# Kernel optimization log

Hardware: AMD Instinct MI355X
Metric: run time of the kernel (lower is better)

## Reference

```python
import jax, jax.numpy as jnp
import numpy as np


def setup_inputs() -> dict:
    key = jax.random.key(0)
    ks = jax.random.split(key, 8)
    B, I, H, O, K = 4096, 512, 512, 512, 16
    s = 0.02
    return {
        "sample": jax.random.normal(ks[0], (B, I), jnp.float32),
        "hiddens": jax.random.normal(ks[1], (K, B, H), jnp.float32),
        "mem_para": jax.random.uniform(ks[2], (B, H), jnp.float32),
        "Wu": jax.random.normal(ks[3], (I + H, H), jnp.float32) * s,
        "bu": jnp.zeros((H,), jnp.float32),
        "Wr": jax.random.normal(ks[4], (I + H, H), jnp.float32) * s,
        "br": jnp.zeros((H,), jnp.float32),
        "Wm": jax.random.normal(ks[5], (I + 2 * H, H), jnp.float32) * s,
        "bm": jnp.zeros((H,), jnp.float32),
        "Wh": jax.random.normal(ks[6], (I + H, H), jnp.float32) * s,
        "bh": jnp.zeros((H,), jnp.float32),
        "Wo": jax.random.normal(ks[7], (H, O), jnp.float32) * s,
        "bo": jnp.zeros((O,), jnp.float32),
    }


def _mem_filter(hiddens, mem_para):
    # hiddens: [k, B, H]; mem_para (memory gate output, 'd'): [B, H]
    # Original per-scalar recurrence: w[k]=1; w[k-1-i] = w[k-i]*(i-d)/(i+1)
    # => w[k-1-i] = cumprod_{m=0..i} (m-d)/(m+1), i.e. signed fractional binomials.
    k = hiddens.shape[0]
    i = jnp.arange(k, dtype=hiddens.dtype)[:, None, None]          # [k,1,1]
    factors = (i - mem_para[None]) / (i + 1.0)                      # [k,B,H]
    weights = jnp.flip(jnp.cumprod(factors, axis=0), axis=0)        # [k,B,H]
    return jnp.sum(hiddens * weights, axis=0)                       # [B,H]


def reference(sample, hiddens, mem_para, Wu, bu, Wr, br, Wm, bm, Wh, bh, Wo, bo):
    hidden = hiddens[-1]                                            # [B,H]
    xh = jnp.concatenate([sample, hidden], axis=1)                  # [B,I+H]
    xhd = jnp.concatenate([xh, mem_para], axis=1)                   # [B,I+2H]
    update_gate = jax.nn.sigmoid(xh @ Wu + bu)
    reset_gate = jax.nn.sigmoid(xh @ Wr + br)
    memory_gate = 0.5 * jax.nn.sigmoid(xhd @ Wm + bm)
    xrh = jnp.concatenate([sample, reset_gate * hidden], axis=1)
    h_tilde = jnp.tanh(xrh @ Wh + bh)
    hiddens_filtered = -_mem_filter(hiddens, memory_gate)
    hidden_now = hiddens_filtered + update_gate * h_tilde           # [B,H]
    updated_hiddens = jnp.concatenate([hiddens[1:], hidden_now[None]], axis=0)
    output = hidden_now @ Wo + bo                                   # [B,O]
    return (output, updated_hiddens, memory_gate)
```

## Files before the change

kernel.cpp:

```cpp
#include <hip/hip_runtime.h>
#include <math.h>

typedef __bf16 bf16;
typedef __bf16 bf16x8 __attribute__((ext_vector_type(8)));
typedef __bf16 bf16x4 __attribute__((ext_vector_type(4)));
typedef float  f32x4  __attribute__((ext_vector_type(4)));

constexpr int BATCH = 4096;
constexpr int HID   = 512;
constexpr int NSTEP = 16;
constexpr int SLICE = BATCH * HID;
constexpr int S4    = SLICE / 4;

__device__ __forceinline__ float sigmoidf_(float x) {
    return 1.0f / (1.0f + __expf(-x));
}
__device__ __forceinline__ float tanh_fast(float x) {
    x = fminf(fmaxf(x, -15.0f), 15.0f);
    float e = __expf(2.0f * x);
    return (e - 1.0f) / (e + 1.0f);
}

__device__ __forceinline__ void gload_lds16(const void* g, void* l) {
    __builtin_amdgcn_global_load_lds((const __attribute__((address_space(1))) void*)g,
                                     (__attribute__((address_space(3))) void*)l,
                                     16, 0, 0);
}

__global__ __launch_bounds__(256)
void prep_all(const float* __restrict__ sample,
              const float* __restrict__ hidden,
              const float* __restrict__ mem_para,
              const float* __restrict__ Wu, const float* __restrict__ Wr,
              const float* __restrict__ Wm, const float* __restrict__ Wh,
              const float* __restrict__ Wo,
              bf16* __restrict__ Sb, bf16* __restrict__ Hb, bf16* __restrict__ Mb,
              bf16* __restrict__ Wall_t, bf16* __restrict__ Wh_t,
              bf16* __restrict__ Wo_t) {
    __shared__ float tile[32][33];
    const int bid = blockIdx.x;
    if (bid < 6144) {
        const int seg = bid >> 11;
        const int i = (bid & 2047) * 256 + threadIdx.x;
        const float* in = (seg == 0) ? sample : (seg == 1) ? hidden : mem_para;
        bf16* out = (seg == 0) ? Sb : (seg == 1) ? Hb : Mb;
        float4 v = ((const float4*)in)[i];
        bf16x4 o = {(bf16)v.x, (bf16)v.y, (bf16)v.z, (bf16)v.w};
        ((bf16x4*)out)[i] = o;
        return;
    }
    const int t = bid - 6144;
    const float* in; bf16* out; int stride, row_off, t2;
    if (t < 512)        { in = Wu; out = Wall_t; stride = 1536; row_off = 0;    t2 = t; }
    else if (t < 1024)  { in = Wr; out = Wall_t; stride = 1536; row_off = 512;  t2 = t - 512; }
    else if (t < 1792)  { in = Wm; out = Wall_t; stride = 1536; row_off = 1024; t2 = t - 1024; }
    else if (t < 2304)  { in = Wh; out = Wh_t;   stride = 1024; row_off = 0;    t2 = t - 1792; }
    else                { in = Wo; out = Wo_t;   stride = 512;  row_off = 0;    t2 = t - 2304; }
    const int r0 = (t2 >> 4) * 32, c0 = (t2 & 15) * 32;
    const int tr = threadIdx.x >> 5;
    const int tc = threadIdx.x & 31;
#pragma unroll
    for (int i = 0; i < 4; ++i)
        tile[tr + i * 8][tc] = in[(size_t)(r0 + tr + i * 8) * 512 + c0 + tc];
    __syncthreads();
#pragma unroll
    for (int i = 0; i < 4; ++i) {
        const int c = tr + i * 8;
        out[(size_t)(row_off + c0 + c) * stride + r0 + tc] = (bf16)tile[tc][c];
    }
}

__global__ __launch_bounds__(256)
void gemm_urm(const bf16* __restrict__ Sb,
              const bf16* __restrict__ Hb,
              const bf16* __restrict__ Mb,
              const bf16* __restrict__ Wall_t,
              const float* __restrict__ bu,
              const float* __restrict__ br,
              const float* __restrict__ bm,
              bf16* __restrict__ UGb,
              bf16* __restrict__ RHb,
              float* __restrict__ out_mg) {
    __shared__ bf16 As[128 * 64];
    __shared__ bf16 Bs[64 * 64];

    const int bid = blockIdx.x;
    const int tid = threadIdx.x;

    const int k8  = bid & 7;
    const int s   = bid >> 3;
    const int colb = s >> 2;
    const int rowb = (k8 << 2) + (s & 3);
    const int brow = rowb * 128;
    const int bcol = colb * 64;

    const int wid  = tid >> 6;
    const int lane = tid & 63;
    const int wr = wid >> 1, wc = wid & 1;

    const bf16* segs[3] = {Sb, Hb, Mb};
    const int nkt = (colb >= 16) ? 24 : 16;

    const int s_row  = tid >> 3;
    const int s_chnk = tid & 7;

    f32x4 acc[4][2] = {};

    for (int t = 0; t < nkt; ++t) {
        const int k0 = t * 64;
        const bf16* Aseg = segs[k0 >> 9];
        const int kloc = k0 & 511;

#pragma unroll
        for (int c = 0; c < 4; ++c) {
            const int row = c * 32 + s_row;
            const int sc  = s_chnk ^ (row & 7);
            gload_lds16(Aseg + (size_t)(brow + row) * 512 + kloc + sc * 8,
                        As + (size_t)(c * 256 + (wid << 6)) * 8);
        }
#pragma unroll
        for (int c = 0; c < 2; ++c) {
            const int row = c * 32 + s_row;
            const int sc  = s_chnk ^ (row & 7);
            gload_lds16(Wall_t + (size_t)(bcol + row) * 1536 + k0 + sc * 8,
                        Bs + (size_t)(c * 256 + (wid << 6)) * 8);
        }
        __syncthreads();

#pragma unroll
        for (int ks = 0; ks < 2; ++ks) {
            const int kb = ks * 64 + ((lane >> 4) << 4);
            bf16x8 bfrag[2];
#pragma unroll
            for (int ni = 0; ni < 2; ++ni) {
                const int n = wc * 32 + ni * 16 + (lane & 15);
                bfrag[ni] = *(const bf16x8*)((const char*)Bs +
                                             n * 128 + (kb ^ ((n & 7) << 4)));
            }
#pragma unroll
            for (int mi = 0; mi < 4; ++mi) {
                const int m = wr * 64 + mi * 16 + (lane & 15);
                const bf16x8 afrag = *(const bf16x8*)((const char*)As +
                                                      m * 128 + (kb ^ ((m & 7) << 4)));
#pragma unroll
                for (int ni = 0; ni < 2; ++ni)
                    acc[mi][ni] = __builtin_amdgcn_mfma_f32_16x16x32_bf16(
                        afrag, bfrag[ni], acc[mi][ni], 0, 0, 0);
            }
        }
        __syncthreads();
    }

    const int lr4 = (lane >> 4) * 4;
    const int lc  = lane & 15;
#pragma unroll
    for (int mi = 0; mi < 4; ++mi) {
#pragma unroll
        for (int ni = 0; ni < 2; ++ni) {
            const int col = bcol + wc * 32 + ni * 16 + lc;
            const f32x4 a = acc[mi][ni];
#pragma unroll
            for (int r = 0; r < 4; ++r) {
                const int row = brow + wr * 64 + mi * 16 + lr4 + r;
                const float x = a[r];
                if (col < 512) {
                    UGb[(size_t)row * 512 + col] = (bf16)sigmoidf_(x + bu[col]);
                } else if (col < 1024) {
                    const int c2 = col - 512;
                    const float v = sigmoidf_(x + br[c2]) *
                                    (float)Hb[(size_t)row * 512 + c2];
                    RHb[(size_t)row * 512 + c2] = (bf16)v;
                } else {
                    const int c3 = col - 1024;
                    out_mg[(size_t)row * 512 + c3] = 0.5f * sigmoidf_(x + bm[c3]);
                }
            }
        }
    }
}

__global__ __launch_bounds__(256)
void gemm_wh_filter(const bf16* __restrict__ Sb,
                    const bf16* __restrict__ RHb,
                    const bf16* __restrict__ Wh_t,
                    const float* __restrict__ bh,
                    bf16* __restrict__ HTb,
                    const float* __restrict__ hiddens,
                    const float* __restrict__ mg,
                    float* __restrict__ out_upd,
                    float* __restrict__ filt) {
    __shared__ bf16 As[128 * 64];
    __shared__ bf16 Bs[64 * 64];

    const int bid = blockIdx.x;
    const int tid = threadIdx.x;

    if (bid >= 256) {
        const int idx = (bid - 256) * 256 + tid;
        const f32x4* h4 = (const f32x4*)hiddens;
        f32x4* o4 = (f32x4*)out_upd;
        const f32x4 d = ((const f32x4*)mg)[idx];
        f32x4 c = {1.f, 1.f, 1.f, 1.f};
        f32x4 a = {0.f, 0.f, 0.f, 0.f};
#pragma unroll
        for (int i = 0; i < NSTEP; ++i) {
            const int j = NSTEP - 1 - i;
            const f32x4 v = h4[(size_t)j * S4 + idx];
            const float fi = (float)i;
            const float inv = 1.0f / (float)(i + 1);
            c *= (fi - d) * inv;
            a += v * c;
            if (j >= 1)
                __builtin_nontemporal_store(v, o4 + (size_t)(j - 1) * S4 + idx);
        }
        ((f32x4*)filt)[idx] = a;
        return;
    }

    const int k8  = bid & 7;
    const int s   = bid >> 3;
    const int colb = s >> 2;
    const int rowb = (k8 << 2) + (s & 3);
    const int brow = rowb * 128;
    const int bcol = colb * 64;

    const int wid  = tid >> 6;
    const int lane = tid & 63;
    const int wr = wid >> 1, wc = wid & 1;

    const bf16* segs[2] = {Sb, RHb};

    const int s_row  = tid >> 3;
    const int s_chnk = tid & 7;

    f32x4 acc[4][2] = {};

    for (int t = 0; t < 16; ++t) {
        const int k0 = t * 64;
        const bf16* Aseg = segs[k0 >> 9];
        const int kloc = k0 & 511;

#pragma unroll
        for (int c = 0; c < 4; ++c) {
            const int row = c * 32 + s_row;
            const int sc  = s_chnk ^ (row & 7);
            gload_lds16(Aseg + (size_t)(brow + row) * 512 + kloc + sc * 8,
                        As + (size_t)(c * 256 + (wid << 6)) * 8);
        }
#pragma unroll
        for (int c = 0; c < 2; ++c) {
            const int row = c * 32 + s_row;
            const int sc  = s_chnk ^ (row & 7);
            gload_lds16(Wh_t + (size_t)(bcol + row) * 1024 + k0 + sc * 8,
                        Bs + (size_t)(c * 256 + (wid << 6)) * 8);
        }
        __syncthreads();

#pragma unroll
        for (int ks = 0; ks < 2; ++ks) {
            const int kb = ks * 64 + ((lane >> 4) << 4);
            bf16x8 bfrag[2];
#pragma unroll
            for (int ni = 0; ni < 2; ++ni) {
                const int n = wc * 32 + ni * 16 + (lane & 15);
                bfrag[ni] = *(const bf16x8*)((const char*)Bs +
                                             n * 128 + (kb ^ ((n & 7) << 4)));
            }
#pragma unroll
            for (int mi = 0; mi < 4; ++mi) {
                const int m = wr * 64 + mi * 16 + (lane & 15);
                const bf16x8 afrag = *(const bf16x8*)((const char*)As +
                                                      m * 128 + (kb ^ ((m & 7) << 4)));
#pragma unroll
                for (int ni = 0; ni < 2; ++ni)
                    acc[mi][ni] = __builtin_amdgcn_mfma_f32_16x16x32_bf16(
                        afrag, bfrag[ni], acc[mi][ni], 0, 0, 0);
            }
        }
        __syncthreads();
    }

    const int lr4 = (lane >> 4) * 4;
    const int lc  = lane & 15;
#pragma unroll
    for (int mi = 0; mi < 4; ++mi) {
#pragma unroll
        for (int ni = 0; ni < 2; ++ni) {
            const int col = bcol + wc * 32 + ni * 16 + lc;
            const f32x4 a = acc[mi][ni];
#pragma unroll
            for (int r = 0; r < 4; ++r) {
                const int row = brow + wr * 64 + mi * 16 + lr4 + r;
                HTb[(size_t)row * 512 + col] = (bf16)tanh_fast(a[r] + bh[col]);
            }
        }
    }
}

__global__ __launch_bounds__(256)
void combine(const float* __restrict__ filt,
             const bf16* __restrict__ ugb,
             const bf16* __restrict__ htb,
             float* __restrict__ out_upd,
             bf16* __restrict__ hnb) {
    const int idx = blockIdx.x * 256 + threadIdx.x;
    const f32x4 a = ((const f32x4*)filt)[idx];
    const bf16x4 u = ((const bf16x4*)ugb)[idx];
    const bf16x4 t = ((const bf16x4*)htb)[idx];
    f32x4 hn;
#pragma unroll
    for (int e = 0; e < 4; ++e)
        hn[e] = fmaf((float)u[e], (float)t[e], -a[e]);
    ((f32x4*)out_upd)[(size_t)(NSTEP - 1) * S4 + idx] = hn;
    bf16x4 hb = {(bf16)hn[0], (bf16)hn[1], (bf16)hn[2], (bf16)hn[3]};
    ((bf16x4*)hnb)[idx] = hb;
}

__global__ __launch_bounds__(256)
void gemm_out(const bf16* __restrict__ HNb,
              const bf16* __restrict__ Wo_t,
              const float* __restrict__ bo,
              float* __restrict__ outp) {
    __shared__ bf16 As[128 * 64];
    __shared__ bf16 Bs[64 * 64];

    const int bid = blockIdx.x;
    const int tid = threadIdx.x;

    const int k8  = bid & 7;
    const int s   = bid >> 3;
    const int colb = s >> 2;
    const int rowb = (k8 << 2) + (s & 3);
    const int brow = rowb * 128;
    const int bcol = colb * 64;

    const int wid  = tid >> 6;
    const int lane = tid & 63;
    const int wr = wid >> 1, wc = wid & 1;

    const int s_row  = tid >> 3;
    const int s_chnk = tid & 7;

    f32x4 acc[4][2] = {};

    for (int t = 0; t < 8; ++t) {
        const int k0 = t * 64;

#pragma unroll
        for (int c = 0; c < 4; ++c) {
            const int row = c * 32 + s_row;
            const int sc  = s_chnk ^ (row & 7);
            gload_lds16(HNb + (size_t)(brow + row) * 512 + k0 + sc * 8,
                        As + (size_t)(c * 256 + (wid << 6)) * 8);
        }
#pragma unroll
        for (int c = 0; c < 2; ++c) {
            const int row = c * 32 + s_row;
            const int sc  = s_chnk ^ (row & 7);
            gload_lds16(Wo_t + (size_t)(bcol + row) * 512 + k0 + sc * 8,
                        Bs + (size_t)(c * 256 + (wid << 6)) * 8);
        }
        __syncthreads();

#pragma unroll
        for (int ks = 0; ks < 2; ++ks) {
            const int kb = ks * 64 + ((lane >> 4) << 4);
            bf16x8 bfrag[2];
#pragma unroll
            for (int ni = 0; ni < 2; ++ni) {
                const int n = wc * 32 + ni * 16 + (lane & 15);
                bfrag[ni] = *(const bf16x8*)((const char*)Bs +
                                             n * 128 + (kb ^ ((n & 7) << 4)));
            }
#pragma unroll
            for (int mi = 0; mi < 4; ++mi) {
                const int m = wr * 64 + mi * 16 + (lane & 15);
                const bf16x8 afrag = *(const bf16x8*)((const char*)As +
                                                      m * 128 + (kb ^ ((m & 7) << 4)));
#pragma unroll
                for (int ni = 0; ni < 2; ++ni)
                    acc[mi][ni] = __builtin_amdgcn_mfma_f32_16x16x32_bf16(
                        afrag, bfrag[ni], acc[mi][ni], 0, 0, 0);
            }
        }
        __syncthreads();
    }

    const int lr4 = (lane >> 4) * 4;
    const int lc  = lane & 15;
#pragma unroll
    for (int mi = 0; mi < 4; ++mi) {
#pragma unroll
        for (int ni = 0; ni < 2; ++ni) {
            const int col = bcol + wc * 32 + ni * 16 + lc;
            const f32x4 a = acc[mi][ni];
#pragma unroll
            for (int r = 0; r < 4; ++r) {
                const int row = brow + wr * 64 + mi * 16 + lr4 + r;
                outp[(size_t)row * 512 + col] = a[r] + bo[col];
            }
        }
    }
}

extern "C" void kernel_launch(void* const* d_in, const int* in_sizes, int n_in,
                              void* d_out, int out_size, void* d_ws, size_t ws_size,
                              hipStream_t stream) {
    const float* sample   = (const float*)d_in[0];
    const float* hiddens  = (const float*)d_in[1];
    const float* mem_para = (const float*)d_in[2];
    const float* Wu = (const float*)d_in[3];
    const float* bu = (const float*)d_in[4];
    const float* Wr = (const float*)d_in[5];
    const float* br = (const float*)d_in[6];
    const float* Wm = (const float*)d_in[7];
    const float* bm = (const float*)d_in[8];
    const float* Wh = (const float*)d_in[9];
    const float* bh = (const float*)d_in[10];
    const float* Wo = (const float*)d_in[11];
    const float* bo = (const float*)d_in[12];

    float* out        = (float*)d_out;
    float* out_output = out;
    float* out_upd    = out + SLICE;
    float* out_mg     = out + SLICE + (size_t)NSTEP * SLICE;

    const float* hidden = hiddens + (size_t)(NSTEP - 1) * SLICE;

    char* ws = (char*)d_ws;
    bf16* Sb    = (bf16*)(ws);
    bf16* Hb    = (bf16*)(ws + (((size_t) 4) << 20));
    bf16* Mb    = (bf16*)(ws + (((size_t) 8) << 20));
    bf16* RHb   = (bf16*)(ws + (((size_t)12) << 20));
    bf16* HNb   = (bf16*)(ws + (((size_t)16) << 20));
    bf16* UGb   = (bf16*)(ws + (((size_t)20) << 20));
    bf16* HTb   = (bf16*)(ws + (((size_t)24) << 20));
    bf16* Wall_t = (bf16*)(ws + (((size_t)28) << 20));
    bf16* Wh_t  = (bf16*)(ws + (((size_t)33) << 20));
    bf16* Wo_t  = (bf16*)(ws + (((size_t)35) << 20));
    float* filt = (float*)(ws + (((size_t)40) << 20));

    dim3 blk(256);

    prep_all<<<8704, blk, 0, stream>>>(sample, hidden, mem_para,
                                       Wu, Wr, Wm, Wh, Wo,
                                       Sb, Hb, Mb, Wall_t, Wh_t, Wo_t);
    gemm_urm<<<768, blk, 0, stream>>>(
        Sb, Hb, Mb, Wall_t, bu, br, bm, UGb, RHb, out_mg);
    gemm_wh_filter<<<256 + 2048, blk, 0, stream>>>(
        Sb, RHb, Wh_t, bh, HTb, hiddens, out_mg, out_upd, filt);
    combine<<<S4 / 256, blk, 0, stream>>>(filt, UGb, HTb, out_upd, HNb);
    gemm_out<<<256, blk, 0, stream>>>(HNb, Wo_t, bo, out_output);
}
```

Measured before the change: 107.8 us.

## Move shifted hidden-state copy into first GEMM launch to overlap with compute

The copy of hiddens[1:] into the updated-hiddens output is moved out of the memory-filter blocks of the second GEMM kernel. It now runs as extra blocks appended to the first gate GEMM launch. The aim is to overlap this large streaming copy with the compute-bound gate GEMM and shorten the filter stage. The cost is that hiddens slices 1..15 are now read twice, once for the copy and once for the filter sum, which adds memory traffic unless it hits in cache.

```diff
diff --git a/kernel.cpp b/kernel.cpp
--- a/kernel.cpp
+++ b/kernel.cpp
@@ -71,21 +71,36 @@
 }
 
 __global__ __launch_bounds__(256)
-void gemm_urm(const bf16* __restrict__ Sb,
-              const bf16* __restrict__ Hb,
-              const bf16* __restrict__ Mb,
-              const bf16* __restrict__ Wall_t,
-              const float* __restrict__ bu,
-              const float* __restrict__ br,
-              const float* __restrict__ bm,
-              bf16* __restrict__ UGb,
-              bf16* __restrict__ RHb,
-              float* __restrict__ out_mg) {
+void gemm_urm_copy(const bf16* __restrict__ Sb,
+                   const bf16* __restrict__ Hb,
+                   const bf16* __restrict__ Mb,
+                   const bf16* __restrict__ Wall_t,
+                   const float* __restrict__ bu,
+                   const float* __restrict__ br,
+                   const float* __restrict__ bm,
+                   bf16* __restrict__ UGb,
+                   bf16* __restrict__ RHb,
+                   float* __restrict__ out_mg,
+                   const float* __restrict__ hiddens,
+                   float* __restrict__ out_upd) {
     __shared__ bf16 As[128 * 64];
     __shared__ bf16 Bs[64 * 64];
 
     const int bid = blockIdx.x;
     const int tid = threadIdx.x;
+
+    if (bid >= 768) {
+        const int base = (bid - 768) * 4096 + tid;
+        const f32x4* src = ((const f32x4*)hiddens) + S4;
+        f32x4* dst = (f32x4*)out_upd;
+#pragma unroll
+        for (int u = 0; u < 16; ++u) {
+            const int f = base + u * 256;
+            f32x4 v = src[f];
+            __builtin_nontemporal_store(v, dst + f);
+        }
+        return;
+    }
 
     const int k8  = bid & 7;
     const int s   = bid >> 3;
@@ -180,15 +195,14 @@
 }
 
 __global__ __launch_bounds__(256)
-void gemm_wh_filter(const bf16* __restrict__ Sb,
-                    const bf16* __restrict__ RHb,
-                    const bf16* __restrict__ Wh_t,
-                    const float* __restrict__ bh,
-                    bf16* __restrict__ HTb,
-                    const float* __restrict__ hiddens,
-                    const float* __restrict__ mg,
-                    float* __restrict__ out_upd,
-                    float* __restrict__ filt) {
+void gemm_wh_sum(const bf16* __restrict__ Sb,
+                 const bf16* __restrict__ RHb,
+                 const bf16* __restrict__ Wh_t,
+                 const float* __restrict__ bh,
+                 bf16* __restrict__ HTb,
+                 const float* __restrict__ hiddens,
+                 const float* __restrict__ mg,
+                 float* __restrict__ filt) {
     __shared__ bf16 As[128 * 64];
     __shared__ bf16 Bs[64 * 64];
 
@@ -197,21 +211,17 @@
 
     if (bid >= 256) {
         const int idx = (bid - 256) * 256 + tid;
-        const f32x4* h4 = (const f32x4*)hiddens;
-        f32x4* o4 = (f32x4*)out_upd;
         const f32x4 d = ((const f32x4*)mg)[idx];
         f32x4 c = {1.f, 1.f, 1.f, 1.f};
         f32x4 a = {0.f, 0.f, 0.f, 0.f};
 #pragma unroll
         for (int i = 0; i < NSTEP; ++i) {
             const int j = NSTEP - 1 - i;
-            const f32x4 v = h4[(size_t)j * S4 + idx];
+            const f32x4 v = ((const f32x4*)hiddens)[(size_t)j * S4 + idx];
             const float fi = (float)i;
             const float inv = 1.0f / (float)(i + 1);
             c *= (fi - d) * inv;
             a += v * c;
-            if (j >= 1)
-                __builtin_nontemporal_store(v, o4 + (size_t)(j - 1) * S4 + idx);
         }
         ((f32x4*)filt)[idx] = a;
         return;
@@ -445,10 +455,10 @@
     prep_all<<<8704, blk, 0, stream>>>(sample, hidden, mem_para,
                                        Wu, Wr, Wm, Wh, Wo,
                                        Sb, Hb, Mb, Wall_t, Wh_t, Wo_t);
-    gemm_urm<<<768, blk, 0, stream>>>(
-        Sb, Hb, Mb, Wall_t, bu, br, bm, UGb, RHb, out_mg);
-    gemm_wh_filter<<<256 + 2048, blk, 0, stream>>>(
-        Sb, RHb, Wh_t, bh, HTb, hiddens, out_mg, out_upd, filt);
+    gemm_urm_copy<<<768 + 1920, blk, 0, stream>>>(
+        Sb, Hb, Mb, Wall_t, bu, br, bm, UGb, RHb, out_mg, hiddens, out_upd);
+    gemm_wh_sum<<<256 + 2048, blk, 0, stream>>>(
+        Sb, RHb, Wh_t, bh, HTb, hiddens, out_mg, filt);
     combine<<<S4 / 256, blk, 0, stream>>>(filt, UGb, HTb, out_upd, HNb);
     gemm_out<<<256, blk, 0, stream>>>(HNb, Wo_t, bo, out_output);
 }
```

After: 123.1 us. +14.2%, slower.

## Move memory filter out of Wh GEMM launch into fused filter-combine kernel

Applied to the files above, without the earlier changes.

The fractional-difference filter and the shift-copy of hiddens move out of the Wh GEMM kernel, where they ran as extra blocks, into the combine kernel. This removes the fp32 `filt` intermediate buffer and its write and read round trip. The streaming loads and stores now use nontemporal hints, and all 16 slices are loaded up front to raise memory-level parallelism. The cost is that the bandwidth-heavy filter no longer overlaps the small 256-block GEMM, and each thread now holds 16 vector registers of loads.

```diff
diff --git a/kernel.cpp b/kernel.cpp
--- a/kernel.cpp
+++ b/kernel.cpp
@@ -180,42 +180,16 @@
 }
 
 __global__ __launch_bounds__(256)
-void gemm_wh_filter(const bf16* __restrict__ Sb,
-                    const bf16* __restrict__ RHb,
-                    const bf16* __restrict__ Wh_t,
-                    const float* __restrict__ bh,
-                    bf16* __restrict__ HTb,
-                    const float* __restrict__ hiddens,
-                    const float* __restrict__ mg,
-                    float* __restrict__ out_upd,
-                    float* __restrict__ filt) {
+void gemm_wh(const bf16* __restrict__ Sb,
+             const bf16* __restrict__ RHb,
+             const bf16* __restrict__ Wh_t,
+             const float* __restrict__ bh,
+             bf16* __restrict__ HTb) {
     __shared__ bf16 As[128 * 64];
     __shared__ bf16 Bs[64 * 64];
 
     const int bid = blockIdx.x;
     const int tid = threadIdx.x;
-
-    if (bid >= 256) {
-        const int idx = (bid - 256) * 256 + tid;
-        const f32x4* h4 = (const f32x4*)hiddens;
-        f32x4* o4 = (f32x4*)out_upd;
-        const f32x4 d = ((const f32x4*)mg)[idx];
-        f32x4 c = {1.f, 1.f, 1.f, 1.f};
-        f32x4 a = {0.f, 0.f, 0.f, 0.f};
-#pragma unroll
-        for (int i = 0; i < NSTEP; ++i) {
-            const int j = NSTEP - 1 - i;
-            const f32x4 v = h4[(size_t)j * S4 + idx];
-            const float fi = (float)i;
-            const float inv = 1.0f / (float)(i + 1);
-            c *= (fi - d) * inv;
-            a += v * c;
-            if (j >= 1)
-                __builtin_nontemporal_store(v, o4 + (size_t)(j - 1) * S4 + idx);
-        }
-        ((f32x4*)filt)[idx] = a;
-        return;
-    }
 
     const int k8  = bid & 7;
     const int s   = bid >> 3;
@@ -298,20 +272,43 @@
 }
 
 __global__ __launch_bounds__(256)
-void combine(const float* __restrict__ filt,
-             const bf16* __restrict__ ugb,
-             const bf16* __restrict__ htb,
-             float* __restrict__ out_upd,
-             bf16* __restrict__ hnb) {
+void filt_comb(const float* __restrict__ hiddens,
+               const float* __restrict__ mg,
+               const bf16* __restrict__ ugb,
+               const bf16* __restrict__ htb,
+               float* __restrict__ out_upd,
+               bf16* __restrict__ hnb) {
     const int idx = blockIdx.x * 256 + threadIdx.x;
-    const f32x4 a = ((const f32x4*)filt)[idx];
+    const f32x4* h4 = (const f32x4*)hiddens;
+    f32x4* o4 = (f32x4*)out_upd;
+
+    f32x4 v[NSTEP];
+#pragma unroll
+    for (int j = 0; j < NSTEP; ++j)
+        v[j] = __builtin_nontemporal_load(h4 + (size_t)j * S4 + idx);
+
+#pragma unroll
+    for (int j = 1; j < NSTEP; ++j)
+        __builtin_nontemporal_store(v[j], o4 + (size_t)(j - 1) * S4 + idx);
+
+    const f32x4 d = __builtin_nontemporal_load(((const f32x4*)mg) + idx);
+    f32x4 c = {1.f, 1.f, 1.f, 1.f};
+    f32x4 a = {0.f, 0.f, 0.f, 0.f};
+#pragma unroll
+    for (int i = 0; i < NSTEP; ++i) {
+        const float fi = (float)i;
+        const float inv = 1.0f / (float)(i + 1);
+        c *= (fi - d) * inv;
+        a += v[NSTEP - 1 - i] * c;
+    }
+
     const bf16x4 u = ((const bf16x4*)ugb)[idx];
     const bf16x4 t = ((const bf16x4*)htb)[idx];
     f32x4 hn;
 #pragma unroll
     for (int e = 0; e < 4; ++e)
         hn[e] = fmaf((float)u[e], (float)t[e], -a[e]);
-    ((f32x4*)out_upd)[(size_t)(NSTEP - 1) * S4 + idx] = hn;
+    __builtin_nontemporal_store(hn, o4 + (size_t)(NSTEP - 1) * S4 + idx);
     bf16x4 hb = {(bf16)hn[0], (bf16)hn[1], (bf16)hn[2], (bf16)hn[3]};
     ((bf16x4*)hnb)[idx] = hb;
 }
@@ -438,7 +435,6 @@
     bf16* Wall_t = (bf16*)(ws + (((size_t)28) << 20));
     bf16* Wh_t  = (bf16*)(ws + (((size_t)33) << 20));
     bf16* Wo_t  = (bf16*)(ws + (((size_t)35) << 20));
-    float* filt = (float*)(ws + (((size_t)40) << 20));
 
     dim3 blk(256);
 
@@ -447,8 +443,8 @@
                                        Sb, Hb, Mb, Wall_t, Wh_t, Wo_t);
     gemm_urm<<<768, blk, 0, stream>>>(
         Sb, Hb, Mb, Wall_t, bu, br, bm, UGb, RHb, out_mg);
-    gemm_wh_filter<<<256 + 2048, blk, 0, stream>>>(
-        Sb, RHb, Wh_t, bh, HTb, hiddens, out_mg, out_upd, filt);
-    combine<<<S4 / 256, blk, 0, stream>>>(filt, UGb, HTb, out_upd, HNb);
+    gemm_wh<<<256, blk, 0, stream>>>(Sb, RHb, Wh_t, bh, HTb);
+    filt_comb<<<S4 / 256, blk, 0, stream>>>(
+        hiddens, out_mg, UGb, HTb, out_upd, HNb);
     gemm_out<<<256, blk, 0, stream>>>(HNb, Wo_t, bo, out_output);
 }
```

After: 126.5 us. 17.3% more time.
